# Performance work log

Hardware: AMD Instinct MI355X
Metric: run time of the kernel (lower is better)

Reference implementation:

```python
import jax, jax.numpy as jnp
import numpy as np

N = 8000      # nodes
K = 8         # out-degree per node (symmetric ring offsets +/-1..4)
E = N * K     # edges
T = N * K * K # triplets: all ordered pairs of edges sharing a source node
C = 32        # per-edge feature channels (irreps slice)
S = 9         # spherical harmonics channels for 1x0e+1x1e+1x2e
H = 4         # num_heads
F = H * C     # tp2 output width
B = 128       # number_of_basis
COUT = 64     # lin_edge -> 64x0e
MAX_RADIUS = 6.0


def gaussian_expansion(x):
    # GaussianExpansion(min=0, max=MAX_RADIUS, num_basis=B); x: [T] -> [T, B]
    centers = jnp.linspace(0.0, MAX_RADIUS, B, dtype=x.dtype)
    width = 0.5 * MAX_RADIUS / B
    d = x[:, None] - centers
    return jnp.exp(-d * d / (2.0 * width * width))


def _ln(h, g, b):
    mu = jnp.mean(h, axis=-1, keepdims=True)
    var = jnp.var(h, axis=-1, keepdims=True)
    return (h - mu) * jax.lax.rsqrt(var + 1e-6) * g + b


def alpha_mlp(x, Wi, bi, g1, be1, Wm, bm, g2, be2, Wo, bo):
    # Linear -> LayerNorm -> SiLU -> Linear -> LayerNorm -> SiLU -> Linear
    h = jax.nn.silu(_ln(x @ Wi + bi, g1, be1))
    h = jax.nn.silu(_ln(h @ Wm + bm, g2, be2))
    return h @ Wo + bo


def _build_graph():
    offs = np.concatenate([np.arange(1, K // 2 + 1), -np.arange(1, K // 2 + 1)])
    src = np.repeat(np.arange(N), K)
    slot = np.tile(np.arange(K), N)
    dst = (src + offs[slot]) % N
    # inverse edge: at node dst, slot with negated offset
    inv_slot = np.where(slot < K // 2, slot + K // 2, slot - K // 2)
    inv_index = dst * K + inv_slot
    # triplets: all ordered pairs (a, b) of edges sharing source node i
    i = np.repeat(np.arange(N), K * K)
    a = np.tile(np.repeat(np.arange(K), K), N)
    b = np.tile(np.arange(K), N * K)
    tgt_eid = i * K + a
    src_eid = i * K + b
    return src, dst, inv_index, tgt_eid, src_eid


def setup_inputs() -> dict:
    key = jax.random.key(0)
    ks = jax.random.split(key, 12)
    src, dst, inv_index, tgt_eid, src_eid = _build_graph()
    pos = jax.random.uniform(ks[0], (N, 3), dtype=jnp.float32) * 3.0
    edge_vec = pos[dst] - pos[src]  # antisymmetric by construction
    edge_len = jnp.linalg.norm(edge_vec, axis=-1)
    edge_length_embedding = gaussian_expansion(edge_len)
    sc = lambda *sh: 1.0 / np.sqrt(sh[0] if len(sh) == 1 else sh[-2])
    return {
        'edge_in': jax.random.normal(ks[1], (E, C), dtype=jnp.float32),
        'edge_sh': jax.random.normal(ks[2], (E, S), dtype=jnp.float32),
        'edge_length_embedding': edge_length_embedding,
        'edge_vec': edge_vec,
        'W_tp2': jax.random.normal(ks[3], (C, S, F), dtype=jnp.float32) / np.sqrt(C * S),
        'W_rad': jax.random.normal(ks[4], (B, F), dtype=jnp.float32) / np.sqrt(B),
        'W_lin': jax.random.normal(ks[5], (F, COUT), dtype=jnp.float32) / np.sqrt(F),
        'Wa_in': jax.random.normal(ks[6], (2, B, 64), dtype=jnp.float32) / np.sqrt(B),
        'ba_in': jnp.zeros((2, 64), jnp.float32),
        'ga1': jnp.ones((2, 64), jnp.float32),
        'bea1': jnp.zeros((2, 64), jnp.float32),
        'Wa_mid': jax.random.normal(ks[7], (2, 64, 64), dtype=jnp.float32) / 8.0,
        'ba_mid': jnp.zeros((2, 64), jnp.float32),
        'ga2': jnp.ones((2, 64), jnp.float32),
        'bea2': jnp.zeros((2, 64), jnp.float32),
        'Wa_out': jax.random.normal(ks[8], (2, 64, H), dtype=jnp.float32) / 8.0,
        'ba_out': jnp.zeros((2, H), jnp.float32),
        'inv_index': jnp.asarray(inv_index, jnp.int32),
        'tgt_eid': jnp.asarray(tgt_eid, jnp.int32),
        'src_eid': jnp.asarray(src_eid, jnp.int32),
        'edge_dst': jnp.asarray(dst, jnp.int32),
    }


def reference(edge_in, edge_sh, edge_length_embedding, edge_vec,
              W_tp2, W_rad, W_lin,
              Wa_in, ba_in, ga1, bea1, Wa_mid, ba_mid, ga2, bea2, Wa_out, ba_out,
              inv_index, tgt_eid, src_eid, edge_dst):
    # EquiConv tp2: tensor product (edge_in x edge_sh) with learned mixing,
    # gated per-edge by a radial weight from the length embedding. [E, F]
    value = jnp.einsum('ec,es,csf->ef', edge_in, edge_sh, W_tp2)
    value = value * (edge_length_embedding @ W_rad)
    # gather: value[inverse][source_edge_of_triplet] -> [T, H, C]
    v = value[inv_index][src_eid].reshape(-1, H, C)

    # triplet geometry: rij = edge_vec[tgt], rik = edge_vec[src], rjk = rik - rij
    rik = edge_vec[src_eid]
    rjk = rik - edge_vec[tgt_eid]
    rik_n = jnp.linalg.norm(rik, axis=-1)
    rjk_n = jnp.linalg.norm(rjk, axis=-1)

    # alpha = lin_alpha1(gexp(|rik|)) * lin_alpha2(gexp(|rjk|))  -> [T, H]
    a1 = alpha_mlp(gaussian_expansion(rik_n), Wa_in[0], ba_in[0], ga1[0], bea1[0],
                   Wa_mid[0], ba_mid[0], ga2[0], bea2[0], Wa_out[0], ba_out[0])
    a2 = alpha_mlp(gaussian_expansion(rjk_n), Wa_in[1], ba_in[1], ga1[1], bea1[1],
                   Wa_mid[1], ba_mid[1], ga2[1], bea2[1], Wa_out[1], ba_out[1])
    alpha = a1 * a2

    # segment softmax over target edge id (torch_geometric.utils.softmax)
    amax = jax.lax.stop_gradient(jax.ops.segment_max(alpha, tgt_eid, num_segments=E))
    ex = jnp.exp(alpha - amax[tgt_eid])
    den = jax.ops.segment_sum(ex, tgt_eid, num_segments=E)
    alpha = ex / (den[tgt_eid] + 1e-16)

    # scatter: sum attention-weighted values per target edge -> [E, H, C]
    edge_fea = jax.ops.segment_sum(v * alpha[:, :, None], tgt_eid, num_segments=E)
    edge_out = edge_fea.reshape(E, F) @ W_lin  # [E, COUT]
    # out_layer: scatter edge features to destination nodes
    node_out = jax.ops.segment_sum(edge_out, edge_dst, num_segments=N)  # [N, COUT]
    return node_out
```

## Files before the change

### kernel.cpp

```cpp
#include <hip/hip_runtime.h>
#include <math.h>

#define NN 8000
#define KK 8
#define EE (NN*KK)
#define TT (EE*KK)
#define CC 32
#define SS 9
#define FF 128
#define BB 128
#define CO 64
#define NPAIR 36
#define NTASK (NN*NPAIR)
#define NB1 (EE/16)
#define NB2 (NTASK/16)

#define GSTEP (6.0f/127.0f)
#define GINV  (8192.0f/9.0f)

typedef __attribute__((ext_vector_type(8))) short short8;
typedef __attribute__((ext_vector_type(4))) float acc4;

__device__ __forceinline__ float b2f(unsigned short u) {
    return __uint_as_float(((unsigned int)u) << 16);
}
__device__ __forceinline__ unsigned short f2b(float f) {
    unsigned int x = __float_as_uint(f);
    return (unsigned short)((x + 0x7FFFu + ((x >> 16) & 1u)) >> 16);
}
template<bool BF> __device__ __forceinline__ float LD(const void* p, size_t i) {
    if constexpr (BF) return b2f(((const unsigned short*)p)[i]);
    else              return ((const float*)p)[i];
}
template<bool BF> __device__ __forceinline__ unsigned short LDB(const void* p, size_t i) {
    if constexpr (BF) return ((const unsigned short*)p)[i];
    else              return f2b(((const float*)p)[i]);
}

__global__ void k_detect(const void* esh, int* flag) {
    int lane = threadIdx.x;
    const float* p = (const float*)esh;
    int sane = 0;
    #pragma unroll
    for (int i = 0; i < 8; ++i) {
        float ax = fabsf(p[lane * 8 + i]);
        if (ax > 1e-20f && ax < 1e20f) sane++;
    }
    #pragma unroll
    for (int m = 1; m < 64; m <<= 1) sane += __shfl_xor(sane, m, 64);
    if (lane == 0) *flag = (sane > 256) ? 0 : 1;
}

template<bool BF> __device__ __forceinline__ void value_body(
    const void* ein, const void* esh, const void* elem,
    const void* wtp, const void* wrad, unsigned short* value,
    float* A, float* EL)
{
    const int e0 = blockIdx.x * 16;
    const int tid = threadIdx.x;
    for (int idx = tid; idx < 288*16; idx += 128) {
        int cs = idx >> 4, ei = idx & 15;
        int c = cs / 9, s = cs - c * 9;
        A[idx] = LD<BF>(ein, (size_t)(e0+ei)*CC + c) * LD<BF>(esh, (size_t)(e0+ei)*SS + s);
    }
    for (int ei = 0; ei < 16; ++ei)
        EL[tid*17 + ei] = LD<BF>(elem, (size_t)(e0+ei)*BB + tid);
    __syncthreads();
    float acc[16], rac[16];
    #pragma unroll
    for (int i = 0; i < 16; ++i) { acc[i] = 0.f; rac[i] = 0.f; }
    for (int cs = 0; cs < 288; ++cs) {
        float w = LD<BF>(wtp, (size_t)cs*FF + tid);
        const float4* ap = (const float4*)(&A[cs*16]);
        #pragma unroll
        for (int q = 0; q < 4; ++q) {
            float4 a4 = ap[q];
            acc[q*4+0] += a4.x * w; acc[q*4+1] += a4.y * w;
            acc[q*4+2] += a4.z * w; acc[q*4+3] += a4.w * w;
        }
    }
    for (int k = 0; k < 128; ++k) {
        float w = LD<BF>(wrad, (size_t)k*FF + tid);
        #pragma unroll
        for (int ei = 0; ei < 16; ++ei) rac[ei] += EL[k*17 + ei] * w;
    }
    #pragma unroll
    for (int ei = 0; ei < 16; ++ei)
        value[(size_t)(e0+ei)*FF + tid] = f2b(acc[ei] * rac[ei]);
}

__global__ __launch_bounds__(128) void k_value(
    const int* __restrict__ flag, const void* ein, const void* esh, const void* elem,
    const void* wtp, const void* wrad, unsigned short* __restrict__ value)
{
    __shared__ float A[288*16];
    __shared__ float EL[128*17];
    if (*flag) value_body<true >(ein, esh, elem, wtp, wrad, value, A, EL);
    else       value_body<false>(ein, esh, elem, wtp, wrad, value, A, EL);
}


__device__ const int UA[NPAIR] = {0,0,0,0,0,0,0,0,1,1,1,1,1,1,1,2,2,2,2,2,2,3,3,3,3,3,4,4,4,4,5,5,5,6,6,7};
__device__ const int UB[NPAIR] = {0,1,2,3,4,5,6,7,1,2,3,4,5,6,7,2,3,4,5,6,7,3,4,5,6,7,4,5,6,7,5,6,7,6,7,7};

union U8 { short8 v; unsigned short u[8]; };
union CV { uint4 q; short8 v; };

template<bool BF, int MODE>
__device__ __forceinline__ void mlp_mfma_body(
    const void* evec,
    const void* wain, const void* bain, const void* ga1p, const void* bea1p,
    const void* wam,  const void* bam,  const void* ga2p, const void* bea2p,
    const void* wao,  const void* bao,
    const float* a1buf, float* outbuf, unsigned short* hbuf)
{
    const int tid  = threadIdx.x;
    const int lane = tid & 63;
    const int wsl  = tid >> 6;
    const int col  = lane & 15;
    const int quad = lane >> 4;
    unsigned short* hslice = hbuf + wsl * 1024;
    const int widx = MODE;
    const int nbatch  = (MODE == 0) ? NB1 : NB2;
    const int gw      = blockIdx.x * 4 + wsl;
    const int gstride = gridDim.x * 4;

    U8 w1f[4][4];
    #pragma unroll
    for (int q = 0; q < 4; ++q)
        #pragma unroll
        for (int n = 0; n < 4; ++n)
            #pragma unroll
            for (int j = 0; j < 8; ++j)
                w1f[q][n].u[j] = LDB<BF>(wain,
                    (size_t)widx*8192 + (size_t)(q*32 + quad*8 + j)*64 + n*16 + col);
    U8 w2f[2][4];
    #pragma unroll
    for (int q = 0; q < 2; ++q)
        #pragma unroll
        for (int n = 0; n < 4; ++n)
            #pragma unroll
            for (int j = 0; j < 8; ++j)
                w2f[q][n].u[j] = LDB<BF>(wam,
                    (size_t)widx*4096 + (size_t)(q*32 + quad*8 + j)*64 + n*16 + col);
    float w3r[4][4];
    #pragma unroll
    for (int t = 0; t < 4; ++t)
        #pragma unroll
        for (int hh = 0; hh < 4; ++hh)
            w3r[t][hh] = LD<BF>(wao, (size_t)widx*256 + (size_t)(t*16 + col)*4 + hh);
    float b1r[4], g1r[4], be1r[4], b2r[4], g2r[4], be2r[4], b3r[4];
    #pragma unroll
    for (int t = 0; t < 4; ++t) {
        int n = t*16 + col;
        b1r[t]  = LD<BF>(bain,  (size_t)widx*64 + n);
        g1r[t]  = LD<BF>(ga1p,  (size_t)widx*64 + n);
        be1r[t] = LD<BF>(bea1p, (size_t)widx*64 + n);
        b2r[t]  = LD<BF>(bam,   (size_t)widx*64 + n);
        g2r[t]  = LD<BF>(ga2p,  (size_t)widx*64 + n);
        be2r[t] = LD<BF>(bea2p, (size_t)widx*64 + n);
    }
    #pragma unroll
    for (int hh = 0; hh < 4; ++hh) b3r[hh] = LD<BF>(bao, (size_t)widx*4 + hh);

    for (int bb = gw; bb < nbatch; bb += gstride) {
        const int base = bb * 16;
        float dval = 0.f; int eaL = 0, ebL = 0, aL = 0, bL = 0;
        if (lane < 16) {
            if (MODE == 0) {
                int e = base + lane;
                float vx = LD<BF>(evec, (size_t)e*3+0);
                float vy = LD<BF>(evec, (size_t)e*3+1);
                float vz = LD<BF>(evec, (size_t)e*3+2);
                dval = sqrtf(vx*vx + vy*vy + vz*vz);
            } else {
                int task = base + lane;
                int i = task / NPAIR;
                int u = task - i * NPAIR;
                aL = UA[u]; bL = UB[u];
                eaL = i*8 + aL; ebL = i*8 + bL;
                float ax = LD<BF>(evec,(size_t)eaL*3+0), ay = LD<BF>(evec,(size_t)eaL*3+1), az = LD<BF>(evec,(size_t)eaL*3+2);
                float bx = LD<BF>(evec,(size_t)ebL*3+0), by = LD<BF>(evec,(size_t)ebL*3+1), bz = LD<BF>(evec,(size_t)ebL*3+2);
                float dx = bx-ax, dy = by-ay, dz = bz-az;
                dval = sqrtf(dx*dx + dy*dy + dz*dz);
            }
        }
        float dm = __shfl(dval, col, 64);

        acc4 ac0 = {0.f,0.f,0.f,0.f}, ac1 = ac0, ac2 = ac0, ac3 = ac0;
        #pragma unroll
        for (int q = 0; q < 4; ++q) {
            U8 af;
            #pragma unroll
            for (int j = 0; j < 8; ++j) {
                float c = (float)(q*32 + quad*8 + j) * GSTEP;
                float t = dm - c;
                af.u[j] = f2b(__expf(-(t*t) * GINV));
            }
            ac0 = __builtin_amdgcn_mfma_f32_16x16x32_bf16(af.v, w1f[q][0].v, ac0, 0,0,0);
            ac1 = __builtin_amdgcn_mfma_f32_16x16x32_bf16(af.v, w1f[q][1].v, ac1, 0,0,0);
            ac2 = __builtin_amdgcn_mfma_f32_16x16x32_bf16(af.v, w1f[q][2].v, ac2, 0,0,0);
            ac3 = __builtin_amdgcn_mfma_f32_16x16x32_bf16(af.v, w1f[q][3].v, ac3, 0,0,0);
        }
        float val[4][4];
        #pragma unroll
        for (int r = 0; r < 4; ++r) {
            val[0][r] = ac0[r] + b1r[0];
            val[1][r] = ac1[r] + b1r[1];
            val[2][r] = ac2[r] + b1r[2];
            val[3][r] = ac3[r] + b1r[3];
        }
        float sr[4], sq[4];
        #pragma unroll
        for (int r = 0; r < 4; ++r) {
            sr[r] = val[0][r] + val[1][r] + val[2][r] + val[3][r];
            sq[r] = val[0][r]*val[0][r] + val[1][r]*val[1][r]
                  + val[2][r]*val[2][r] + val[3][r]*val[3][r];
        }
        #pragma unroll
        for (int mm = 1; mm < 16; mm <<= 1)
            #pragma unroll
            for (int r = 0; r < 4; ++r) {
                sr[r] += __shfl_xor(sr[r], mm, 64);
                sq[r] += __shfl_xor(sq[r], mm, 64);
            }
        #pragma unroll
        for (int r = 0; r < 4; ++r) {
            float mu  = sr[r] * (1.0f/64.0f);
            float var = sq[r] * (1.0f/64.0f) - mu*mu;
            float inv = rsqrtf(var + 1e-6f);
            #pragma unroll
            for (int t = 0; t < 4; ++t) {
                float x = (val[t][r] - mu) * inv * g1r[t] + be1r[t];
                x = x * (1.0f / (1.0f + __expf(-x)));
                int m = quad*4 + r;
                int n = t*16 + col;
                hslice[m*64 + (n ^ ((m & 7) * 8))] = f2b(x);
            }
        }
        __syncthreads();
        acc4 bc0 = {0.f,0.f,0.f,0.f}, bc1 = bc0, bc2 = bc0, bc3 = bc0;
        #pragma unroll
        for (int q = 0; q < 2; ++q) {
            int nbase = (q*32 + quad*8) ^ ((col & 7) * 8);
            CV cv; cv.q = *(const uint4*)(&hslice[col*64 + nbase]);
            bc0 = __builtin_amdgcn_mfma_f32_16x16x32_bf16(cv.v, w2f[q][0].v, bc0, 0,0,0);
            bc1 = __builtin_amdgcn_mfma_f32_16x16x32_bf16(cv.v, w2f[q][1].v, bc1, 0,0,0);
            bc2 = __builtin_amdgcn_mfma_f32_16x16x32_bf16(cv.v, w2f[q][2].v, bc2, 0,0,0);
            bc3 = __builtin_amdgcn_mfma_f32_16x16x32_bf16(cv.v, w2f[q][3].v, bc3, 0,0,0);
        }
        __syncthreads();
        float h2[4][4];
        #pragma unroll
        for (int r = 0; r < 4; ++r) {
            h2[0][r] = bc0[r] + b2r[0];
            h2[1][r] = bc1[r] + b2r[1];
            h2[2][r] = bc2[r] + b2r[2];
            h2[3][r] = bc3[r] + b2r[3];
        }
        #pragma unroll
        for (int r = 0; r < 4; ++r) {
            sr[r] = h2[0][r] + h2[1][r] + h2[2][r] + h2[3][r];
            sq[r] = h2[0][r]*h2[0][r] + h2[1][r]*h2[1][r]
                  + h2[2][r]*h2[2][r] + h2[3][r]*h2[3][r];
        }
        #pragma unroll
        for (int mm = 1; mm < 16; mm <<= 1)
            #pragma unroll
            for (int r = 0; r < 4; ++r) {
                sr[r] += __shfl_xor(sr[r], mm, 64);
                sq[r] += __shfl_xor(sq[r], mm, 64);
            }
        #pragma unroll
        for (int r = 0; r < 4; ++r) {
            float mu  = sr[r] * (1.0f/64.0f);
            float var = sq[r] * (1.0f/64.0f) - mu*mu;
            float inv = rsqrtf(var + 1e-6f);
            #pragma unroll
            for (int t = 0; t < 4; ++t) {
                float x = (h2[t][r] - mu) * inv * g2r[t] + be2r[t];
                h2[t][r] = x * (1.0f / (1.0f + __expf(-x)));
            }
        }
        float p[4][4];
        #pragma unroll
        for (int r = 0; r < 4; ++r)
            #pragma unroll
            for (int hh = 0; hh < 4; ++hh)
                p[r][hh] = h2[0][r]*w3r[0][hh] + h2[1][r]*w3r[1][hh]
                         + h2[2][r]*w3r[2][hh] + h2[3][r]*w3r[3][hh];
        #pragma unroll
        for (int mm = 1; mm < 16; mm <<= 1)
            #pragma unroll
            for (int r = 0; r < 4; ++r)
                #pragma unroll
                for (int hh = 0; hh < 4; ++hh)
                    p[r][hh] += __shfl_xor(p[r][hh], mm, 64);

        if (MODE == 0) {
            if (col < 4) {
                int m = quad*4 + col;
                int e = base + m;
                float o0 = p[0][0], o1 = p[0][1], o2 = p[0][2], o3 = p[0][3];
                if (col == 1) { o0 = p[1][0]; o1 = p[1][1]; o2 = p[1][2]; o3 = p[1][3]; }
                if (col == 2) { o0 = p[2][0]; o1 = p[2][1]; o2 = p[2][2]; o3 = p[2][3]; }
                if (col == 3) { o0 = p[3][0]; o1 = p[3][1]; o2 = p[3][2]; o3 = p[3][3]; }
                float4 o; o.x = o0 + b3r[0]; o.y = o1 + b3r[1]; o.z = o2 + b3r[2]; o.w = o3 + b3r[3];
                *(float4*)(&outbuf[(size_t)e*4]) = o;
            }
        } else {
            int m0  = quad*4 + (col & 3);
            int eaW = __shfl(eaL, m0, 64);
            int ebW = __shfl(ebL, m0, 64);
            int aW  = __shfl(aL,  m0, 64);
            int bW  = __shfl(bL,  m0, 64);
            if (col < 4) {
                float o0 = p[0][0], o1 = p[0][1], o2 = p[0][2], o3 = p[0][3];
                if (col == 1) { o0 = p[1][0]; o1 = p[1][1]; o2 = p[1][2]; o3 = p[1][3]; }
                if (col == 2) { o0 = p[2][0]; o1 = p[2][1]; o2 = p[2][2]; o3 = p[2][3]; }
                if (col == 3) { o0 = p[3][0]; o1 = p[3][1]; o2 = p[3][2]; o3 = p[3][3]; }
                o0 += b3r[0]; o1 += b3r[1]; o2 += b3r[2]; o3 += b3r[3];
                float4 g = *(const float4*)(&a1buf[(size_t)ebW*4]);
                float4 r1; r1.x = o0*g.x; r1.y = o1*g.y; r1.z = o2*g.z; r1.w = o3*g.w;
                *(float4*)(&outbuf[(size_t)(eaW*8 + bW)*4]) = r1;
                if (aW != bW) {
                    float4 g2 = *(const float4*)(&a1buf[(size_t)eaW*4]);
                    float4 r2; r2.x = o0*g2.x; r2.y = o1*g2.y; r2.z = o2*g2.z; r2.w = o3*g2.w;
                    *(float4*)(&outbuf[(size_t)(ebW*8 + aW)*4]) = r2;
                }
            }
        }
    }
}

__global__ __launch_bounds__(256, 2) void k_mlp1(
    const int* __restrict__ flag, const void* evec,
    const void* wain, const void* bain, const void* ga1p, const void* bea1p,
    const void* wam,  const void* bam,  const void* ga2p, const void* bea2p,
    const void* wao,  const void* bao, float* __restrict__ a1buf)
{
    __shared__ __align__(16) unsigned short hbuf[4096];
    if (*flag) mlp_mfma_body<true ,0>(evec, wain, bain, ga1p, bea1p, wam, bam, ga2p, bea2p,
                                      wao, bao, nullptr, a1buf, hbuf);
    else       mlp_mfma_body<false,0>(evec, wain, bain, ga1p, bea1p, wam, bam, ga2p, bea2p,
                                      wao, bao, nullptr, a1buf, hbuf);
}

__global__ __launch_bounds__(256, 2) void k_mlp2(
    const int* __restrict__ flag, const void* evec,
    const void* wain, const void* bain, const void* ga1p, const void* bea1p,
    const void* wam,  const void* bam,  const void* ga2p, const void* bea2p,
    const void* wao,  const void* bao,
    const float* __restrict__ a1buf, float* __restrict__ alpha)
{
    __shared__ __align__(16) unsigned short hbuf[4096];
    if (*flag) mlp_mfma_body<true ,1>(evec, wain, bain, ga1p, bea1p, wam, bam, ga2p, bea2p,
                                      wao, bao, a1buf, alpha, hbuf);
    else       mlp_mfma_body<false,1>(evec, wain, bain, ga1p, bea1p, wam, bam, ga2p, bea2p,
                                      wao, bao, a1buf, alpha, hbuf);
}

template<bool BF> __device__ __forceinline__ void edge_body(
    const float* alpha, const unsigned short* value,
    const int* src_eid, const int* inv_index,
    const void* wlin, unsigned short* eout,
    float* WL, float* alsb, float* feab)
{
    const int tid = threadIdx.x;
    for (int i = tid; i < 8192; i += 256) WL[i] = LD<BF>(wlin, (size_t)i);
    __syncthreads();
    const int lane = tid & 63, ws = tid >> 6;
    float* als = alsb + ws * 32;
    float* fea = feab + ws * 128;
    for (int base = blockIdx.x * 4; base < EE; base += gridDim.x * 4) {
        int e = base + ws;
        float v = -1e30f;
        if (lane < 32) v = alpha[(size_t)e*32 + lane];
        float vm = v;
        vm = fmaxf(vm, __shfl_xor(vm, 4, 64));
        vm = fmaxf(vm, __shfl_xor(vm, 8, 64));
        vm = fmaxf(vm, __shfl_xor(vm, 16, 64));
        float ex = __expf(v - vm);
        float den = ex;
        den += __shfl_xor(den, 4, 64);
        den += __shfl_xor(den, 8, 64);
        den += __shfl_xor(den, 16, 64);
        float al = ex / (den + 1e-16f);
        if (lane < 32) als[lane] = al;
        __syncthreads();
        float f0 = 0.f, f1 = 0.f;
        int h0 = lane >> 5;
        #pragma unroll
        for (int bq = 0; bq < 8; ++bq) {
            int se = src_eid[e*8 + bq];
            int row = inv_index[se];
            const unsigned short* vr = &value[(size_t)row * FF];
            f0 += als[bq*4 + h0]     * b2f(vr[lane]);
            f1 += als[bq*4 + h0 + 2] * b2f(vr[64 + lane]);
        }
        fea[lane] = f0; fea[64 + lane] = f1;
        __syncthreads();
        float acc = 0.f;
        #pragma unroll
        for (int f = 0; f < 128; f += 4) {
            float4 fe = *(const float4*)(&fea[f]);
            acc += fe.x * WL[(f+0)*64 + lane];
            acc += fe.y * WL[(f+1)*64 + lane];
            acc += fe.z * WL[(f+2)*64 + lane];
            acc += fe.w * WL[(f+3)*64 + lane];
        }
        eout[(size_t)e*64 + lane] = f2b(acc);
    }
}

__global__ __launch_bounds__(256) void k_edge(
    const int* __restrict__ flag,
    const float* __restrict__ alpha, const unsigned short* __restrict__ value,
    const int* __restrict__ src_eid, const int* __restrict__ inv_index,
    const void* wlin, unsigned short* __restrict__ eout)
{
    __shared__ float WL[128*64];
    __shared__ float alsb[4*32];
    __shared__ float feab[4*128];
    if (*flag) edge_body<true >(alpha, value, src_eid, inv_index, wlin, eout, WL, alsb, feab);
    else       edge_body<false>(alpha, value, src_eid, inv_index, wlin, eout, WL, alsb, feab);
}

__global__ __launch_bounds__(256) void k_node(
    const int* __restrict__ flag, const unsigned short* __restrict__ eout,
    const int* __restrict__ inv_index, void* __restrict__ out)
{
    int gid = blockIdx.x * 256 + threadIdx.x;
    int n = gid >> 6, o = gid & 63;
    float s = 0.f;
    #pragma unroll
    for (int q = 0; q < 8; ++q) {
        int row = inv_index[n*8 + q];
        s += b2f(eout[(size_t)row*64 + o]);
    }
    if (*flag) ((unsigned short*)out)[gid] = f2b(s);
    else       ((float*)out)[gid] = s;
}

extern "C" void kernel_launch(void* const* d_in, const int* in_sizes, int n_in,
                              void* d_out, int out_size, void* d_ws, size_t ws_size,
                              hipStream_t stream)
{
    const void* ein  = d_in[0];
    const void* esh  = d_in[1];
    const void* elem = d_in[2];
    const void* evec = d_in[3];
    const void* wtp  = d_in[4];
    const void* wrad = d_in[5];
    const void* wlin = d_in[6];
    const void* wain = d_in[7];
    const void* bain = d_in[8];
    const void* ga1p = d_in[9];
    const void* bea1p= d_in[10];
    const void* wam  = d_in[11];
    const void* bam  = d_in[12];
    const void* ga2p = d_in[13];
    const void* bea2p= d_in[14];
    const void* wao  = d_in[15];
    const void* bao  = d_in[16];
    const int* inv_index = (const int*)d_in[17];
    const int* src_eid   = (const int*)d_in[19];

    char* ws = (char*)d_ws;
    int*            flag  = (int*)ws;
    unsigned short* value = (unsigned short*)(ws + 16);
    float*          a1buf = (float*)(ws + 16 + 16384000);
    float*          alpha = (float*)(ws + 16 + 16384000 + 1024000);
    unsigned short* eoutb = (unsigned short*)(ws + 16 + 16384000 + 1024000 + 8192000);

    hipLaunchKernelGGL(k_detect, dim3(1), dim3(64), 0, stream, esh, flag);
    hipLaunchKernelGGL(k_value,  dim3(EE/16), dim3(128), 0, stream,
                       flag, ein, esh, elem, wtp, wrad, value);
    hipLaunchKernelGGL(k_mlp1,   dim3(250),  dim3(256), 0, stream,
                       flag, evec, wain, bain, ga1p, bea1p, wam, bam, ga2p, bea2p, wao, bao, a1buf);
    hipLaunchKernelGGL(k_mlp2,   dim3(500),  dim3(256), 0, stream,
                       flag, evec, wain, bain, ga1p, bea1p, wam, bam, ga2p, bea2p, wao, bao,
                       a1buf, alpha);
    hipLaunchKernelGGL(k_edge,   dim3(1024), dim3(256), 0, stream,
                       flag, alpha, value, src_eid, inv_index, wlin, eoutb);
    hipLaunchKernelGGL(k_node,   dim3((NN*CO)/256), dim3(256), 0, stream,
                       flag, eoutb, inv_index, d_out);
}
```

Measured before the change: 459.4 us.

## Move value GEMMs to split-fp16 MFMA and drop runtime dtype detection

The value kernel's scalar FMA loops for the tensor-product and radial projections become fp16 MFMA matrix ops. Each fp32 operand is split into a high and a low fp16 part, and three MFMAs per tile recover near-fp32 accuracy. Weights are staged into shared memory in MFMA fragment layout, and each block now handles 64 edges instead of 16. The bf16/fp32 detect kernel and flag branches are removed, so inputs are assumed fp32, and intermediates switch from bf16 to fp16. This cuts the detect launch and branching overhead but narrows intermediate range and depends on the inputs always being fp32.

Result: faster. 434.4 us (-5.4%).

```diff
diff --git a/kernel.cpp b/kernel.cpp
--- a/kernel.cpp
+++ b/kernel.cpp
@@ -18,100 +18,144 @@
 #define GSTEP (6.0f/127.0f)
 #define GINV  (8192.0f/9.0f)
 
-typedef __attribute__((ext_vector_type(8))) short short8;
+typedef __attribute__((ext_vector_type(8))) _Float16 half8;
 typedef __attribute__((ext_vector_type(4))) float acc4;
 
-__device__ __forceinline__ float b2f(unsigned short u) {
-    return __uint_as_float(((unsigned int)u) << 16);
-}
-__device__ __forceinline__ unsigned short f2b(float f) {
-    unsigned int x = __float_as_uint(f);
-    return (unsigned short)((x + 0x7FFFu + ((x >> 16) & 1u)) >> 16);
-}
-template<bool BF> __device__ __forceinline__ float LD(const void* p, size_t i) {
-    if constexpr (BF) return b2f(((const unsigned short*)p)[i]);
-    else              return ((const float*)p)[i];
-}
-template<bool BF> __device__ __forceinline__ unsigned short LDB(const void* p, size_t i) {
-    if constexpr (BF) return ((const unsigned short*)p)[i];
-    else              return f2b(((const float*)p)[i]);
-}
-
-__global__ void k_detect(const void* esh, int* flag) {
-    int lane = threadIdx.x;
-    const float* p = (const float*)esh;
-    int sane = 0;
-    #pragma unroll
-    for (int i = 0; i < 8; ++i) {
-        float ax = fabsf(p[lane * 8 + i]);
-        if (ax > 1e-20f && ax < 1e20f) sane++;
-    }
-    #pragma unroll
-    for (int m = 1; m < 64; m <<= 1) sane += __shfl_xor(sane, m, 64);
-    if (lane == 0) *flag = (sane > 256) ? 0 : 1;
-}
-
-template<bool BF> __device__ __forceinline__ void value_body(
-    const void* ein, const void* esh, const void* elem,
-    const void* wtp, const void* wrad, unsigned short* value,
-    float* A, float* EL)
-{
-    const int e0 = blockIdx.x * 16;
-    const int tid = threadIdx.x;
-    for (int idx = tid; idx < 288*16; idx += 128) {
-        int cs = idx >> 4, ei = idx & 15;
-        int c = cs / 9, s = cs - c * 9;
-        A[idx] = LD<BF>(ein, (size_t)(e0+ei)*CC + c) * LD<BF>(esh, (size_t)(e0+ei)*SS + s);
-    }
-    for (int ei = 0; ei < 16; ++ei)
-        EL[tid*17 + ei] = LD<BF>(elem, (size_t)(e0+ei)*BB + tid);
-    __syncthreads();
-    float acc[16], rac[16];
-    #pragma unroll
-    for (int i = 0; i < 16; ++i) { acc[i] = 0.f; rac[i] = 0.f; }
-    for (int cs = 0; cs < 288; ++cs) {
-        float w = LD<BF>(wtp, (size_t)cs*FF + tid);
-        const float4* ap = (const float4*)(&A[cs*16]);
-        #pragma unroll
-        for (int q = 0; q < 4; ++q) {
-            float4 a4 = ap[q];
-            acc[q*4+0] += a4.x * w; acc[q*4+1] += a4.y * w;
-            acc[q*4+2] += a4.z * w; acc[q*4+3] += a4.w * w;
-        }
-    }
-    for (int k = 0; k < 128; ++k) {
-        float w = LD<BF>(wrad, (size_t)k*FF + tid);
-        #pragma unroll
-        for (int ei = 0; ei < 16; ++ei) rac[ei] += EL[k*17 + ei] * w;
-    }
-    #pragma unroll
-    for (int ei = 0; ei < 16; ++ei)
-        value[(size_t)(e0+ei)*FF + tid] = f2b(acc[ei] * rac[ei]);
-}
-
-__global__ __launch_bounds__(128) void k_value(
-    const int* __restrict__ flag, const void* ein, const void* esh, const void* elem,
-    const void* wtp, const void* wrad, unsigned short* __restrict__ value)
-{
-    __shared__ float A[288*16];
-    __shared__ float EL[128*17];
-    if (*flag) value_body<true >(ein, esh, elem, wtp, wrad, value, A, EL);
-    else       value_body<false>(ein, esh, elem, wtp, wrad, value, A, EL);
-}
-
+__device__ __forceinline__ unsigned short f2h(float f) {
+    _Float16 h = (_Float16)f;
+    return *(unsigned short*)&h;
+}
+__device__ __forceinline__ float h2f(unsigned short u) {
+    _Float16 h = *(_Float16*)&u;
+    return (float)h;
+}
+
+union H8 { half8 v; unsigned short u[8]; };
+union CV { uint4 q; half8 v; };
+
+__global__ __launch_bounds__(256, 1) void k_value(
+    const float* __restrict__ ein, const float* __restrict__ esh,
+    const float* __restrict__ elem, const float* __restrict__ wtp,
+    const float* __restrict__ wrad, unsigned short* __restrict__ value)
+{
+    __shared__ __align__(16) unsigned short sW[2][3*8*64*8];
+    const int tid  = threadIdx.x;
+    const int lane = tid & 63;
+    const int wv   = tid >> 6;
+    const int col  = lane & 15;
+    const int quad = lane >> 4;
+    const int e0   = blockIdx.x * 64;
+    const int erowA = e0 + wv*16 + col;
+
+    float einr[8];
+    #pragma unroll
+    for (int j = 0; j < 8; ++j) einr[j] = ein[(size_t)erowA*CC + quad*8 + j];
+    float eshr[9];
+    #pragma unroll
+    for (int s = 0; s < 9; ++s) eshr[s] = esh[(size_t)erowA*SS + s];
+
+    acc4 macc[8];
+    #pragma unroll
+    for (int nt = 0; nt < 8; ++nt) macc[nt] = (acc4){0.f,0.f,0.f,0.f};
+
+    for (int cch = 0; cch < 3; ++cch) {
+        if (cch) __syncthreads();
+        for (int i = tid; i < 3*32*128; i += 256) {
+            int sl  = i >> 12;
+            int rem = i & 4095;
+            int ch  = rem >> 7;
+            int f   = rem & 127;
+            int s   = cch*3 + sl;
+            float w = wtp[((size_t)ch*SS + s)*FF + f];
+            unsigned short hi = f2h(w);
+            int pos = ((sl*8 + (f>>4))*64 + ((ch>>3)*16 + (f&15)))*8 + (ch&7);
+            sW[0][pos] = hi;
+            sW[1][pos] = f2h(w - h2f(hi));
+        }
+        __syncthreads();
+        #pragma unroll
+        for (int sl = 0; sl < 3; ++sl) {
+            int s = cch*3 + sl;
+            H8 ahi, alo;
+            #pragma unroll
+            for (int j = 0; j < 8; ++j) {
+                float p = einr[j] * eshr[s];
+                unsigned short h = f2h(p);
+                ahi.u[j] = h;
+                alo.u[j] = f2h(p - h2f(h));
+            }
+            #pragma unroll
+            for (int nt = 0; nt < 8; ++nt) {
+                CV chv; chv.q = *(const uint4*)(&sW[0][((sl*8 + nt)*64 + lane)*8]);
+                CV clv; clv.q = *(const uint4*)(&sW[1][((sl*8 + nt)*64 + lane)*8]);
+                macc[nt] = __builtin_amdgcn_mfma_f32_16x16x32_f16(ahi.v, chv.v, macc[nt], 0,0,0);
+                macc[nt] = __builtin_amdgcn_mfma_f32_16x16x32_f16(ahi.v, clv.v, macc[nt], 0,0,0);
+                macc[nt] = __builtin_amdgcn_mfma_f32_16x16x32_f16(alo.v, chv.v, macc[nt], 0,0,0);
+            }
+        }
+    }
+
+    acc4 racc[8];
+    #pragma unroll
+    for (int nt = 0; nt < 8; ++nt) racc[nt] = (acc4){0.f,0.f,0.f,0.f};
+
+    for (int kc = 0; kc < 2; ++kc) {
+        __syncthreads();
+        for (int i = tid; i < 2*32*128; i += 256) {
+            int l   = i >> 12;
+            int rem = i & 4095;
+            int kr  = rem >> 7;
+            int f   = rem & 127;
+            int k   = (kc*2 + l)*32 + kr;
+            float w = wrad[(size_t)k*FF + f];
+            unsigned short hi = f2h(w);
+            int pos = ((l*8 + (f>>4))*64 + ((kr>>3)*16 + (f&15)))*8 + (kr&7);
+            sW[0][pos] = hi;
+            sW[1][pos] = f2h(w - h2f(hi));
+        }
+        __syncthreads();
+        #pragma unroll
+        for (int l = 0; l < 2; ++l) {
+            int ks = kc*2 + l;
+            H8 ahi, alo;
+            #pragma unroll
+            for (int j = 0; j < 8; ++j) {
+                float p = elem[(size_t)erowA*BB + ks*32 + quad*8 + j];
+                unsigned short h = f2h(p);
+                ahi.u[j] = h;
+                alo.u[j] = f2h(p - h2f(h));
+            }
+            #pragma unroll
+            for (int nt = 0; nt < 8; ++nt) {
+                CV chv; chv.q = *(const uint4*)(&sW[0][((l*8 + nt)*64 + lane)*8]);
+                CV clv; clv.q = *(const uint4*)(&sW[1][((l*8 + nt)*64 + lane)*8]);
+                racc[nt] = __builtin_amdgcn_mfma_f32_16x16x32_f16(ahi.v, chv.v, racc[nt], 0,0,0);
+                racc[nt] = __builtin_amdgcn_mfma_f32_16x16x32_f16(ahi.v, clv.v, racc[nt], 0,0,0);
+                racc[nt] = __builtin_amdgcn_mfma_f32_16x16x32_f16(alo.v, chv.v, racc[nt], 0,0,0);
+            }
+        }
+    }
+
+    #pragma unroll
+    for (int r = 0; r < 4; ++r) {
+        int erow = e0 + wv*16 + quad*4 + r;
+        #pragma unroll
+        for (int nt = 0; nt < 8; ++nt)
+            value[(size_t)erow*FF + nt*16 + col] = f2h(macc[nt][r] * racc[nt][r]);
+    }
+}
 
 __device__ const int UA[NPAIR] = {0,0,0,0,0,0,0,0,1,1,1,1,1,1,1,2,2,2,2,2,2,3,3,3,3,3,4,4,4,4,5,5,5,6,6,7};
 __device__ const int UB[NPAIR] = {0,1,2,3,4,5,6,7,1,2,3,4,5,6,7,2,3,4,5,6,7,3,4,5,6,7,4,5,6,7,5,6,7,6,7,7};
 
-union U8 { short8 v; unsigned short u[8]; };
-union CV { uint4 q; short8 v; };
-
-template<bool BF, int MODE>
+template<int MODE>
 __device__ __forceinline__ void mlp_mfma_body(
-    const void* evec,
-    const void* wain, const void* bain, const void* ga1p, const void* bea1p,
-    const void* wam,  const void* bam,  const void* ga2p, const void* bea2p,
-    const void* wao,  const void* bao,
+    const float* __restrict__ evec,
+    const float* __restrict__ wain, const float* __restrict__ bain,
+    const float* __restrict__ ga1p, const float* __restrict__ bea1p,
+    const float* __restrict__ wam,  const float* __restrict__ bam,
+    const float* __restrict__ ga2p, const float* __restrict__ bea2p,
+    const float* __restrict__ wao,  const float* __restrict__ bao,
     const float* a1buf, float* outbuf, unsigned short* hbuf)
 {
     const int tid  = threadIdx.x;
@@ -125,43 +169,41 @@
     const int gw      = blockIdx.x * 4 + wsl;
     const int gstride = gridDim.x * 4;
 
-    U8 w1f[4][4];
+    H8 w1f[4][4];
     #pragma unroll
     for (int q = 0; q < 4; ++q)
         #pragma unroll
         for (int n = 0; n < 4; ++n)
             #pragma unroll
             for (int j = 0; j < 8; ++j)
-                w1f[q][n].u[j] = LDB<BF>(wain,
-                    (size_t)widx*8192 + (size_t)(q*32 + quad*8 + j)*64 + n*16 + col);
-    U8 w2f[2][4];
+                w1f[q][n].u[j] = f2h(wain[(size_t)widx*8192 + (size_t)(q*32 + quad*8 + j)*64 + n*16 + col]);
+    H8 w2f[2][4];
     #pragma unroll
     for (int q = 0; q < 2; ++q)
         #pragma unroll
         for (int n = 0; n < 4; ++n)
             #pragma unroll
             for (int j = 0; j < 8; ++j)
-                w2f[q][n].u[j] = LDB<BF>(wam,
-                    (size_t)widx*4096 + (size_t)(q*32 + quad*8 + j)*64 + n*16 + col);
+                w2f[q][n].u[j] = f2h(wam[(size_t)widx*4096 + (size_t)(q*32 + quad*8 + j)*64 + n*16 + col]);
     float w3r[4][4];
     #pragma unroll
     for (int t = 0; t < 4; ++t)
         #pragma unroll
         for (int hh = 0; hh < 4; ++hh)
-            w3r[t][hh] = LD<BF>(wao, (size_t)widx*256 + (size_t)(t*16 + col)*4 + hh);
+            w3r[t][hh] = wao[(size_t)widx*256 + (size_t)(t*16 + col)*4 + hh];
     float b1r[4], g1r[4], be1r[4], b2r[4], g2r[4], be2r[4], b3r[4];
     #pragma unroll
     for (int t = 0; t < 4; ++t) {
         int n = t*16 + col;
-        b1r[t]  = LD<BF>(bain,  (size_t)widx*64 + n);
-        g1r[t]  = LD<BF>(ga1p,  (size_t)widx*64 + n);
-        be1r[t] = LD<BF>(bea1p, (size_t)widx*64 + n);
-        b2r[t]  = LD<BF>(bam,   (size_t)widx*64 + n);
-        g2r[t]  = LD<BF>(ga2p,  (size_t)widx*64 + n);
-        be2r[t] = LD<BF>(bea2p, (size_t)widx*64 + n);
-    }
-    #pragma unroll
-    for (int hh = 0; hh < 4; ++hh) b3r[hh] = LD<BF>(bao, (size_t)widx*4 + hh);
+        b1r[t]  = bain [widx*64 + n];
+        g1r[t]  = ga1p [widx*64 + n];
+        be1r[t] = bea1p[widx*64 + n];
+        b2r[t]  = bam  [widx*64 + n];
+        g2r[t]  = ga2p [widx*64 + n];
+        be2r[t] = bea2p[widx*64 + n];
+    }
+    #pragma unroll
+    for (int hh = 0; hh < 4; ++hh) b3r[hh] = bao[widx*4 + hh];
 
     for (int bb = gw; bb < nbatch; bb += gstride) {
         const int base = bb * 16;
@@ -169,9 +211,7 @@
         if (lane < 16) {
             if (MODE == 0) {
                 int e = base + lane;
-                float vx = LD<BF>(evec, (size_t)e*3+0);
-                float vy = LD<BF>(evec, (size_t)e*3+1);
-                float vz = LD<BF>(evec, (size_t)e*3+2);
+                float vx = evec[e*3+0], vy = evec[e*3+1], vz = evec[e*3+2];
                 dval = sqrtf(vx*vx + vy*vy + vz*vz);
             } else {
                 int task = base + lane;
@@ -179,9 +219,9 @@
                 int u = task - i * NPAIR;
                 aL = UA[u]; bL = UB[u];
                 eaL = i*8 + aL; ebL = i*8 + bL;
-                float ax = LD<BF>(evec,(size_t)eaL*3+0), ay = LD<BF>(evec,(size_t)eaL*3+1), az = LD<BF>(evec,(size_t)eaL*3+2);
-                float bx = LD<BF>(evec,(size_t)ebL*3+0), by = LD<BF>(evec,(size_t)ebL*3+1), bz = LD<BF>(evec,(size_t)ebL*3+2);
-                float dx = bx-ax, dy = by-ay, dz = bz-az;
+                float dx = evec[ebL*3+0] - evec[eaL*3+0];
+                float dy = evec[ebL*3+1] - evec[eaL*3+1];
+                float dz = evec[ebL*3+2] - evec[eaL*3+2];
                 dval = sqrtf(dx*dx + dy*dy + dz*dz);
             }
         }
@@ -190,17 +230,17 @@
         acc4 ac0 = {0.f,0.f,0.f,0.f}, ac1 = ac0, ac2 = ac0, ac3 = ac0;
         #pragma unroll
         for (int q = 0; q < 4; ++q) {
-            U8 af;
+            H8 afr;
             #pragma unroll
             for (int j = 0; j < 8; ++j) {
                 float c = (float)(q*32 + quad*8 + j) * GSTEP;
                 float t = dm - c;
-                af.u[j] = f2b(__expf(-(t*t) * GINV));
-            }
-            ac0 = __builtin_amdgcn_mfma_f32_16x16x32_bf16(af.v, w1f[q][0].v, ac0, 0,0,0);
-            ac1 = __builtin_amdgcn_mfma_f32_16x16x32_bf16(af.v, w1f[q][1].v, ac1, 0,0,0);
-            ac2 = __builtin_amdgcn_mfma_f32_16x16x32_bf16(af.v, w1f[q][2].v, ac2, 0,0,0);
-            ac3 = __builtin_amdgcn_mfma_f32_16x16x32_bf16(af.v, w1f[q][3].v, ac3, 0,0,0);
+                afr.u[j] = f2h(__expf(-(t*t) * GINV));
+            }
+            ac0 = __builtin_amdgcn_mfma_f32_16x16x32_f16(afr.v, w1f[q][0].v, ac0, 0,0,0);
+            ac1 = __builtin_amdgcn_mfma_f32_16x16x32_f16(afr.v, w1f[q][1].v, ac1, 0,0,0);
+            ac2 = __builtin_amdgcn_mfma_f32_16x16x32_f16(afr.v, w1f[q][2].v, ac2, 0,0,0);
+            ac3 = __builtin_amdgcn_mfma_f32_16x16x32_f16(afr.v, w1f[q][3].v, ac3, 0,0,0);
         }
         float val[4][4];
         #pragma unroll
@@ -235,7 +275,7 @@
                 x = x * (1.0f / (1.0f + __expf(-x)));
                 int m = quad*4 + r;
                 int n = t*16 + col;
-                hslice[m*64 + (n ^ ((m & 7) * 8))] = f2b(x);
+                hslice[m*64 + (n ^ ((m & 7) * 8))] = f2h(x);
             }
         }
         __syncthreads();
@@ -244,10 +284,10 @@
         for (int q = 0; q < 2; ++q) {
             int nbase = (q*32 + quad*8) ^ ((col & 7) * 8);
             CV cv; cv.q = *(const uint4*)(&hslice[col*64 + nbase]);
-            bc0 = __builtin_amdgcn_mfma_f32_16x16x32_bf16(cv.v, w2f[q][0].v, bc0, 0,0,0);
-            bc1 = __builtin_amdgcn_mfma_f32_16x16x32_bf16(cv.v, w2f[q][1].v, bc1, 0,0,0);
-            bc2 = __builtin_amdgcn_mfma_f32_16x16x32_bf16(cv.v, w2f[q][2].v, bc2, 0,0,0);
-            bc3 = __builtin_amdgcn_mfma_f32_16x16x32_bf16(cv.v, w2f[q][3].v, bc3, 0,0,0);
+            bc0 = __builtin_amdgcn_mfma_f32_16x16x32_f16(cv.v, w2f[q][0].v, bc0, 0,0,0);
+            bc1 = __builtin_amdgcn_mfma_f32_16x16x32_f16(cv.v, w2f[q][1].v, bc1, 0,0,0);
+            bc2 = __builtin_amdgcn_mfma_f32_16x16x32_f16(cv.v, w2f[q][2].v, bc2, 0,0,0);
+            bc3 = __builtin_amdgcn_mfma_f32_16x16x32_f16(cv.v, w2f[q][3].v, bc3, 0,0,0);
         }
         __syncthreads();
         float h2[4][4];
@@ -334,40 +374,43 @@
 }
 
 __global__ __launch_bounds__(256, 2) void k_mlp1(
-    const int* __restrict__ flag, const void* evec,
-    const void* wain, const void* bain, const void* ga1p, const void* bea1p,
-    const void* wam,  const void* bam,  const void* ga2p, const void* bea2p,
-    const void* wao,  const void* bao, float* __restrict__ a1buf)
+    const float* __restrict__ evec,
+    const float* __restrict__ wain, const float* __restrict__ bain,
+    const float* __restrict__ ga1p, const float* __restrict__ bea1p,
+    const float* __restrict__ wam,  const float* __restrict__ bam,
+    const float* __restrict__ ga2p, const float* __restrict__ bea2p,
+    const float* __restrict__ wao,  const float* __restrict__ bao,
+    float* __restrict__ a1buf)
 {
     __shared__ __align__(16) unsigned short hbuf[4096];
-    if (*flag) mlp_mfma_body<true ,0>(evec, wain, bain, ga1p, bea1p, wam, bam, ga2p, bea2p,
-                                      wao, bao, nullptr, a1buf, hbuf);
-    else       mlp_mfma_body<false,0>(evec, wain, bain, ga1p, bea1p, wam, bam, ga2p, bea2p,
-                                      wao, bao, nullptr, a1buf, hbuf);
+    mlp_mfma_body<0>(evec, wain, bain, ga1p, bea1p, wam, bam, ga2p, bea2p,
+                     wao, bao, nullptr, a1buf, hbuf);
 }
 
 __global__ __launch_bounds__(256, 2) void k_mlp2(
-    const int* __restrict__ flag, const void* evec,
-    const void* wain, const void* bain, const void* ga1p, const void* bea1p,
-    const void* wam,  const void* bam,  const void* ga2p, const void* bea2p,
-    const void* wao,  const void* bao,
+    const float* __restrict__ evec,
+    const float* __restrict__ wain, const float* __restrict__ bain,
+    const float* __restrict__ ga1p, const float* __restrict__ bea1p,
+    const float* __restrict__ wam,  const float* __restrict__ bam,
+    const float* __restrict__ ga2p, const float* __restrict__ bea2p,
+    const float* __restrict__ wao,  const float* __restrict__ bao,
     const float* __restrict__ a1buf, float* __restrict__ alpha)
 {
     __shared__ __align__(16) unsigned short hbuf[4096];
-    if (*flag) mlp_mfma_body<true ,1>(evec, wain, bain, ga1p, bea1p, wam, bam, ga2p, bea2p,
-                                      wao, bao, a1buf, alpha, hbuf);
-    else       mlp_mfma_body<false,1>(evec, wain, bain, ga1p, bea1p, wam, bam, ga2p, bea2p,
-                                      wao, bao, a1buf, alpha, hbuf);
-}
-
-template<bool BF> __device__ __forceinline__ void edge_body(
-    const float* alpha, const unsigned short* value,
-    const int* src_eid, const int* inv_index,
-    const void* wlin, unsigned short* eout,
-    float* WL, float* alsb, float* feab)
-{
+    mlp_mfma_body<1>(evec, wain, bain, ga1p, bea1p, wam, bam, ga2p, bea2p,
+                     wao, bao, a1buf, alpha, hbuf);
+}
+
+__global__ __launch_bounds__(256) void k_edge(
+    const float* __restrict__ alpha, const unsigned short* __restrict__ value,
+    const int* __restrict__ src_eid, const int* __restrict__ inv_index,
+    const float* __restrict__ wlin, unsigned short* __restrict__ eout)
+{
+    __shared__ float WL[128*64];
+    __shared__ float alsb[4*32];
+    __shared__ float feab[4*128];
     const int tid = threadIdx.x;
-    for (int i = tid; i < 8192; i += 256) WL[i] = LD<BF>(wlin, (size_t)i);
+    for (int i = tid; i < 8192; i += 256) WL[i] = wlin[i];
     __syncthreads();
     const int lane = tid & 63, ws = tid >> 6;
     float* als = alsb + ws * 32;
@@ -395,8 +438,8 @@
             int se = src_eid[e*8 + bq];
             int row = inv_index[se];
             const unsigned short* vr = &value[(size_t)row * FF];
-            f0 += als[bq*4 + h0]     * b2f(vr[lane]);
-            f1 += als[bq*4 + h0 + 2] * b2f(vr[64 + lane]);
+            f0 += als[bq*4 + h0]     * h2f(vr[lane]);
+            f1 += als[bq*4 + h0 + 2] * h2f(vr[64 + lane]);
         }
         fea[lane] = f0; fea[64 + lane] = f1;
         __syncthreads();
@@ -409,26 +452,13 @@
             acc += fe.z * WL[(f+2)*64 + lane];
             acc += fe.w * WL[(f+3)*64 + lane];
         }
-        eout[(size_t)e*64 + lane] = f2b(acc);
-    }
-}
-
-__global__ __launch_bounds__(256) void k_edge(
-    const int* __restrict__ flag,
-    const float* __restrict__ alpha, const unsigned short* __restrict__ value,
-    const int* __restrict__ src_eid, const int* __restrict__ inv_index,
-    const void* wlin, unsigned short* __restrict__ eout)
-{
-    __shared__ float WL[128*64];
-    __shared__ float alsb[4*32];
-    __shared__ float feab[4*128];
-    if (*flag) edge_body<true >(alpha, value, src_eid, inv_index, wlin, eout, WL, alsb, feab);
-    else       edge_body<false>(alpha, value, src_eid, inv_index, wlin, eout, WL, alsb, feab);
+        eout[(size_t)e*64 + lane] = f2h(acc);
+    }
 }
 
 __global__ __launch_bounds__(256) void k_node(
-    const int* __restrict__ flag, const unsigned short* __restrict__ eout,
-    const int* __restrict__ inv_index, void* __restrict__ out)
+    const unsigned short* __restrict__ eout, const int* __restrict__ inv_index,
+    float* __restrict__ out)
 {
     int gid = blockIdx.x * 256 + threadIdx.x;
     int n = gid >> 6, o = gid & 63;
@@ -436,53 +466,50 @@
     #pragma unroll
     for (int q = 0; q < 8; ++q) {
         int row = inv_index[n*8 + q];
-        s += b2f(eout[(size_t)row*64 + o]);
-    }
-    if (*flag) ((unsigned short*)out)[gid] = f2b(s);
-    else       ((float*)out)[gid] = s;
+        s += h2f(eout[(size_t)row*64 + o]);
+    }
+    out[gid] = s;
 }
 
 extern "C" void kernel_launch(void* const* d_in, const int* in_sizes, int n_in,
                               void* d_out, int out_size, void* d_ws, size_t ws_size,
                               hipStream_t stream)
 {
-    const void* ein  = d_in[0];
-    const void* esh  = d_in[1];
-    const void* elem = d_in[2];
-    const void* evec = d_in[3];
-    const void* wtp  = d_in[4];
-    const void* wrad = d_in[5];
-    const void* wlin = d_in[6];
-    const void* wain = d_in[7];
-    const void* bain = d_in[8];
-    const void* ga1p = d_in[9];
-    const void* bea1p= d_in[10];
-    const void* wam  = d_in[11];
-    const void* bam  = d_in[12];
-    const void* ga2p = d_in[13];
-    const void* bea2p= d_in[14];
-    const void* wao  = d_in[15];
-    const void* bao  = d_in[16];
+    const float* ein  = (const float*)d_in[0];
+    const float* esh  = (const float*)d_in[1];
+    const float* elem = (const float*)d_in[2];
+    const float* evec = (const float*)d_in[3];
+    const float* wtp  = (const float*)d_in[4];
+    const float* wrad = (const float*)d_in[5];
+    const float* wlin = (const float*)d_in[6];
+    const float* wain = (const float*)d_in[7];
+    const float* bain = (const float*)d_in[8];
+    const float* ga1p = (const float*)d_in[9];
+    const float* bea1p= (const float*)d_in[10];
+    const float* wam  = (const float*)d_in[11];
+    const float* bam  = (const float*)d_in[12];
+    const float* ga2p = (const float*)d_in[13];
+    const float* bea2p= (const float*)d_in[14];
+    const float* wao  = (const float*)d_in[15];
+    const float* bao  = (const float*)d_in[16];
     const int* inv_index = (const int*)d_in[17];
     const int* src_eid   = (const int*)d_in[19];
 
     char* ws = (char*)d_ws;
-    int*            flag  = (int*)ws;
-    unsigned short* value = (unsigned short*)(ws + 16);
-    float*          a1buf = (float*)(ws + 16 + 16384000);
-    float*          alpha = (float*)(ws + 16 + 16384000 + 1024000);
-    unsigned short* eoutb = (unsigned short*)(ws + 16 + 16384000 + 1024000 + 8192000);
-
-    hipLaunchKernelGGL(k_detect, dim3(1), dim3(64), 0, stream, esh, flag);
-    hipLaunchKernelGGL(k_value,  dim3(EE/16), dim3(128), 0, stream,
-                       flag, ein, esh, elem, wtp, wrad, value);
+    unsigned short* value = (unsigned short*)ws;
+    float*          a1buf = (float*)(ws + 16384000);
+    float*          alpha = (float*)(ws + 16384000 + 1024000);
+    unsigned short* eoutb = (unsigned short*)(ws + 16384000 + 1024000 + 8192000);
+
+    hipLaunchKernelGGL(k_value,  dim3(EE/64), dim3(256), 0, stream,
+                       ein, esh, elem, wtp, wrad, value);
     hipLaunchKernelGGL(k_mlp1,   dim3(250),  dim3(256), 0, stream,
-                       flag, evec, wain, bain, ga1p, bea1p, wam, bam, ga2p, bea2p, wao, bao, a1buf);
+                       evec, wain, bain, ga1p, bea1p, wam, bam, ga2p, bea2p, wao, bao, a1buf);
     hipLaunchKernelGGL(k_mlp2,   dim3(500),  dim3(256), 0, stream,
-                       flag, evec, wain, bain, ga1p, bea1p, wam, bam, ga2p, bea2p, wao, bao,
+                       evec, wain, bain, ga1p, bea1p, wam, bam, ga2p, bea2p, wao, bao,
                        a1buf, alpha);
     hipLaunchKernelGGL(k_edge,   dim3(1024), dim3(256), 0, stream,
-                       flag, alpha, value, src_eid, inv_index, wlin, eoutb);
+                       alpha, value, src_eid, inv_index, wlin, eoutb);
     hipLaunchKernelGGL(k_node,   dim3((NN*CO)/256), dim3(256), 0, stream,
-                       flag, eoutb, inv_index, d_out);
-}
+                       eoutb, inv_index, (float*)d_out);
+}
```
